# Performance work log

Measured on AMD Instinct MI355X. Metric: run time of the kernel, lower is better.

## Reference

```python
import jax, jax.numpy as jnp
import numpy as np

INPUT_DIM = 1024
LATENT_DIM = 1024


def setup_inputs() -> dict:
    key = jax.random.key(0)
    ks = jax.random.split(key, 8)
    B, T = 64, 512
    concat_dim = INPUT_DIM + LATENT_DIM
    s = lambda fan_in: 1.0 / np.sqrt(fan_in)
    return {
        "x": jax.random.normal(ks[0], (B, T, INPUT_DIM), dtype=jnp.float32),
        "h0": jax.random.normal(ks[1], (B, LATENT_DIM), dtype=jnp.float32),
        "w_W": jax.random.uniform(ks[2], (concat_dim, 2 * LATENT_DIM), jnp.float32, -s(concat_dim), s(concat_dim)),
        "w_b": jax.random.uniform(ks[3], (2 * LATENT_DIM,), jnp.float32, -s(concat_dim), s(concat_dim)),
        "wx_W": jax.random.uniform(ks[4], (INPUT_DIM, LATENT_DIM), jnp.float32, -s(INPUT_DIM), s(INPUT_DIM)),
        "wx_b": jax.random.uniform(ks[5], (LATENT_DIM,), jnp.float32, -s(INPUT_DIM), s(INPUT_DIM)),
        "wh_W": jax.random.uniform(ks[6], (LATENT_DIM, LATENT_DIM), jnp.float32, -s(LATENT_DIM), s(LATENT_DIM)),
        "wh_b": jax.random.uniform(ks[7], (LATENT_DIM,), jnp.float32, -s(LATENT_DIM), s(LATENT_DIM)),
    }


def reference(x, h0, w_W, w_b, wx_W, wx_b, wh_W, wh_b):
    # x: [B, T, D_in] (batch_first). Scan over time.
    xT = jnp.swapaxes(x, 0, 1)  # [T, B, D_in]

    def step(h, x_t):
        # fused gate: sigmoid(cat([x,h]) @ W + b) -> chunk into hidden/output gates
        fused = jax.nn.sigmoid(jnp.concatenate([x_t, h], axis=-1) @ w_W + w_b)
        hidden_state, output_state = jnp.split(fused, 2, axis=-1)
        memory_state = (x_t @ wx_W + wx_b) + hidden_state * (h @ wh_W + wh_b)
        h_new = output_state * h + (1.0 - output_state) * jnp.tanh(memory_state)
        return h_new, h_new

    _, hs = jax.lax.scan(step, h0, xT)  # hs: [T, B, L]
    return jnp.swapaxes(hs, 0, 1)  # [B, T, L]
```

## Files before the change

kernel.cpp:

```cpp
#include <hip/hip_runtime.h>
#include <hip/hip_bf16.h>


typedef __attribute__((ext_vector_type(4))) int   int4v;
typedef __attribute__((ext_vector_type(4))) short short4v;
typedef __attribute__((ext_vector_type(8))) short bf16x8;
typedef __attribute__((ext_vector_type(4))) float f32x4;

union Pack16 { int4v i; short4v s[2]; };
union FragU  { bf16x8 v; short4v s[2]; int4v i; };

__device__ __forceinline__ short f2bf(float f) {
  union { float f; unsigned u; } v; v.f = f;
  unsigned r = v.u + 0x7fffu + ((v.u >> 16) & 1u);
  return (short)(r >> 16);
}
__device__ __forceinline__ float bf2f(short s) {
  union { unsigned u; float f; } v; v.u = ((unsigned)(unsigned short)s) << 16;
  return v.f;
}

#define LDS_BARRIER()                                         \
  do {                                                        \
    asm volatile("s_waitcnt lgkmcnt(0)" ::: "memory");        \
    __builtin_amdgcn_s_barrier();                             \
    asm volatile("" ::: "memory");                            \
  } while (0)

__device__ __forceinline__ void gload_lds16(const short* g, short* l) {
  __builtin_amdgcn_global_load_lds(
      (const __attribute__((address_space(1))) void*)g,
      (__attribute__((address_space(3))) void*)l, 16, 0, 0);
}


__global__ __launch_bounds__(256) void cast_x_kernel(const float* __restrict__ xf,
                                                     short* __restrict__ xbf, int n4) {
  int i = blockIdx.x * 256 + threadIdx.x;
  if (i < n4) {
    float4 v = ((const float4*)xf)[i];
    short4v o;
    o.x = f2bf(v.x); o.y = f2bf(v.y); o.z = f2bf(v.z); o.w = f2bf(v.w);
    int r_in = i >> 8, c = i & 255;
    int b = r_in >> 9, t = r_in & 511;
    ((short4v*)xbf)[((t << 6) + b) * 256 + c] = o;
  }
}

__global__ __launch_bounds__(256) void transpose_cast(const float* __restrict__ src,
                                                      long ld, short* __restrict__ dst) {
  __shared__ float tile[64][65];
  const int n0 = blockIdx.x << 6, k0 = blockIdx.y << 6;
  const int c = threadIdx.x & 63, rr = threadIdx.x >> 6;
#pragma unroll 4
  for (int i = 0; i < 16; ++i)
    tile[i * 4 + rr][c] = src[(long)(k0 + i * 4 + rr) * ld + n0 + c];
  __syncthreads();
#pragma unroll 4
  for (int i = 0; i < 16; ++i)
    dst[(long)(n0 + i * 4 + rr) * 1024 + k0 + c] = f2bf(tile[c][i * 4 + rr]);
}

__global__ __launch_bounds__(256) void prep_misc(const float* __restrict__ wb,
                                                 const float* __restrict__ wxb,
                                                 const float* __restrict__ h0,
                                                 float* __restrict__ biasP,
                                                 short* __restrict__ hbf0) {
  int i = blockIdx.x * 256 + threadIdx.x;
  if (i < 65536) {
    hbf0[i] = f2bf(h0[i]);
  } else {
    int n = i - 65536;
    if (n < 3072) biasP[n] = (n < 2048) ? wb[n] : wxb[n - 2048];
  }
}

__global__ __launch_bounds__(256) void pgemm_kernel(const short* __restrict__ A,
                                                    const short* __restrict__ Bt,
                                                    const float* __restrict__ biasP,
                                                    short* __restrict__ P) {
  __shared__ short As[128][32];
  __shared__ short Bs[128][32];
  const int tid = threadIdx.x;
  const int m0 = blockIdx.y << 7;
  const int n0 = blockIdx.x << 7;
  const int w = tid >> 6, lane = tid & 63;
  const int wm = w >> 1, wn = w & 1;
  const int q = lane >> 4, r = lane & 15;

  const int srow = (w << 5) + (lane >> 2);
  const int scol = (lane & 3) * 8;
  const short* gA0 = A  + (long)(m0 + srow) * 1024 + scol;
  const short* gA1 = gA0 + 16 * 1024;
  const short* gB0 = Bt + (long)(n0 + srow) * 1024 + scol;
  const short* gB1 = gB0 + 16 * 1024;
  short* lA0 = &As[(w << 5)][0];
  short* lA1 = &As[(w << 5) + 16][0];
  short* lB0 = &Bs[(w << 5)][0];
  short* lB1 = &Bs[(w << 5) + 16][0];

  const f32x4 zero = {0.f, 0.f, 0.f, 0.f};
  f32x4 acc[4][4];
#pragma unroll
  for (int a = 0; a < 4; ++a)
#pragma unroll
    for (int b = 0; b < 4; ++b) acc[a][b] = zero;

  for (int kk = 0; kk < 1024; kk += 32) {
    gload_lds16(gA0 + kk, lA0);
    gload_lds16(gA1 + kk, lA1);
    gload_lds16(gB0 + kk, lB0);
    gload_lds16(gB1 + kk, lB1);
    __syncthreads();

    FragU af[4], bfv[4];
#pragma unroll
    for (int mi = 0; mi < 4; ++mi)
      af[mi].i = *(const int4v*)&As[wm * 64 + mi * 16 + r][q * 8];
#pragma unroll
    for (int ni = 0; ni < 4; ++ni)
      bfv[ni].i = *(const int4v*)&Bs[wn * 64 + ni * 16 + r][q * 8];
#pragma unroll
    for (int mi = 0; mi < 4; ++mi)
#pragma unroll
      for (int ni = 0; ni < 4; ++ni)
        acc[mi][ni] = __builtin_amdgcn_mfma_f32_16x16x32_bf16(af[mi].v, bfv[ni].v,
                                                              acc[mi][ni], 0, 0, 0);
    __syncthreads();
  }

#pragma unroll
  for (int ni = 0; ni < 4; ++ni) {
    int gn = n0 + wn * 64 + ni * 16 + r;
    float bias = biasP[gn];
#pragma unroll
    for (int mi = 0; mi < 4; ++mi) {
      int gm = m0 + wm * 64 + mi * 16 + q * 4;
#pragma unroll
      for (int i = 0; i < 4; ++i)
        P[(long)(gm + i) * 3072 + gn] = f2bf(acc[mi][ni][i] + bias);
    }
  }
}

__global__ __launch_bounds__(256, 1) void recur_kernel(const short* __restrict__ RT,
                                                       const short* __restrict__ P,
                                                       const float* __restrict__ whb,
                                                       const float* __restrict__ h0,
                                                       short* __restrict__ hbuf,
                                                       float* __restrict__ out,
                                                       unsigned* __restrict__ sync) {
  __shared__ float Lred[4][3][256];
  __shared__ unsigned long long hstage_u[32];
  short* hstage = (short*)hstage_u;

  const int tid = threadIdx.x;
  const int bid = blockIdx.x;
  const int cg = bid & 63, bg = bid >> 6;
  const int w = tid >> 6, lane = tid & 63;
  const int q = lane >> 4, r = lane & 15;
  const int ks = w << 8;
  const f32x4 zero = {0.f, 0.f, 0.f, 0.f};

  FragU Bf[3][8];
#pragma unroll
  for (int nt = 0; nt < 3; ++nt)
#pragma unroll
    for (int ki = 0; ki < 8; ++ki) {
      const short* p = RT + (long)(nt * 1024 + cg * 16 + r) * 1024 + ks + ki * 32 + q * 8;
      Pack16 t16; t16.i = *(const int4v*)p;
      Bf[nt][ki].s[0] = t16.s[0]; Bf[nt][ki].s[1] = t16.s[1];
    }

  const int bl = tid >> 4, jl = tid & 15;
  float hp = h0[(long)(bg * 16 + bl) * 1024 + cg * 16 + jl];
  const float whbr = whb[cg * 16 + jl];
  const short* Pbase = P + (long)(bg * 16 + bl) * 3072 + cg * 16 + jl;
  short p0n = Pbase[0], p1n = Pbase[1024], p2n = Pbase[2048];
  const long outbase = ((long)(bg * 16 + bl) * 512) * 1024 + cg * 16 + jl;

  unsigned* ctr = sync + bg * 32;
  unsigned* gf  = sync + 128 + bg * 32;

  for (int t = 0; t < 512; ++t) {
    const short* hcur = hbuf + (t & 1) * 65536;
    short* hnext = hbuf + ((t + 1) & 1) * 65536;

    const short* aptr = hcur + (bg * 16 + r) * 1024 + ks + q * 8;
    FragU Af[8];
    asm volatile(
        "global_load_dwordx4 %0, %8, off sc0 sc1\n\t"
        "global_load_dwordx4 %1, %8, off offset:64 sc0 sc1\n\t"
        "global_load_dwordx4 %2, %8, off offset:128 sc0 sc1\n\t"
        "global_load_dwordx4 %3, %8, off offset:192 sc0 sc1\n\t"
        "global_load_dwordx4 %4, %8, off offset:256 sc0 sc1\n\t"
        "global_load_dwordx4 %5, %8, off offset:320 sc0 sc1\n\t"
        "global_load_dwordx4 %6, %8, off offset:384 sc0 sc1\n\t"
        "global_load_dwordx4 %7, %8, off offset:448 sc0 sc1\n\t"
        "s_waitcnt vmcnt(0)"
        : "=&v"(Af[0].i), "=&v"(Af[1].i), "=&v"(Af[2].i), "=&v"(Af[3].i),
          "=&v"(Af[4].i), "=&v"(Af[5].i), "=&v"(Af[6].i), "=&v"(Af[7].i)
        : "v"(aptr)
        : "memory");

    short c0 = p0n, c1 = p1n, c2 = p2n;
    if (t < 511) {
      const short* Pn = Pbase + (long)(t + 1) * 196608;
      p0n = Pn[0]; p1n = Pn[1024]; p2n = Pn[2048];
    }

    f32x4 acc0 = zero, acc1 = zero, acc2 = zero;
#pragma unroll
    for (int ki = 0; ki < 8; ++ki) {
      acc0 = __builtin_amdgcn_mfma_f32_16x16x32_bf16(Af[ki].v, Bf[0][ki].v, acc0, 0, 0, 0);
      acc1 = __builtin_amdgcn_mfma_f32_16x16x32_bf16(Af[ki].v, Bf[1][ki].v, acc1, 0, 0, 0);
      acc2 = __builtin_amdgcn_mfma_f32_16x16x32_bf16(Af[ki].v, Bf[2][ki].v, acc2, 0, 0, 0);
    }

#pragma unroll
    for (int i = 0; i < 4; ++i) {
      Lred[w][0][(q * 4 + i) * 16 + r] = acc0[i];
      Lred[w][1][(q * 4 + i) * 16 + r] = acc1[i];
      Lred[w][2][(q * 4 + i) * 16 + r] = acc2[i];
    }
    LDS_BARRIER();

    float g0 = Lred[0][0][tid] + Lred[1][0][tid] + Lred[2][0][tid] + Lred[3][0][tid];
    float g1 = Lred[0][1][tid] + Lred[1][1][tid] + Lred[2][1][tid] + Lred[3][1][tid];
    float g2 = Lred[0][2][tid] + Lred[1][2][tid] + Lred[2][2][tid] + Lred[3][2][tid];

    float gh = 1.f / (1.f + __expf(-(bf2f(c0) + g0)));
    float go = 1.f / (1.f + __expf(-(bf2f(c1) + g1)));
    float mem = bf2f(c2) + gh * (g2 + whbr);
    float e = __expf(2.f * mem);
    float th = 1.f - 2.f / (e + 1.f);
    float hn = go * hp + (1.f - go) * th;
    hp = hn;
    out[outbase + (long)t * 1024] = hn;
    hstage[tid] = f2bf(hn);
    LDS_BARRIER();

    if (tid < 64) {
      int row = bg * 16 + (tid >> 2);
      unsigned long long* hp64 = (unsigned long long*)(hnext + row * 1024 + cg * 16 + (tid & 3) * 4);
      __hip_atomic_store(hp64, hstage_u[tid], __ATOMIC_RELAXED, __HIP_MEMORY_SCOPE_AGENT);
      asm volatile("s_waitcnt vmcnt(0)" ::: "memory");
      if (tid == 0) {
        unsigned old = __hip_atomic_fetch_add(ctr, 1u, __ATOMIC_RELAXED,
                                              __HIP_MEMORY_SCOPE_AGENT);
        if (old == 64u * (unsigned)(t + 1) - 1u)
          __hip_atomic_store(gf, (unsigned)(t + 1), __ATOMIC_RELAXED,
                             __HIP_MEMORY_SCOPE_AGENT);
      }
      while (__hip_atomic_load(gf, __ATOMIC_RELAXED, __HIP_MEMORY_SCOPE_AGENT) <
             (unsigned)(t + 1))
        __builtin_amdgcn_s_sleep(1);
    }
    LDS_BARRIER();
  }
}


extern "C" void kernel_launch(void* const* d_in, const int* in_sizes, int n_in,
                              void* d_out, int out_size, void* d_ws, size_t ws_size,
                              hipStream_t stream) {
  const float* x   = (const float*)d_in[0];
  const float* h0  = (const float*)d_in[1];
  const float* wW  = (const float*)d_in[2];
  const float* wb  = (const float*)d_in[3];
  const float* wxW = (const float*)d_in[4];
  const float* wxb = (const float*)d_in[5];
  const float* whW = (const float*)d_in[6];
  const float* whb = (const float*)d_in[7];
  float* out = (float*)d_out;

  char* ws = (char*)d_ws;
  short*    P     = (short*)(ws);
  short*    xbf   = (short*)(ws + 201326592);
  short*    XwT   = (short*)(ws + 268435456);
  short*    RT    = (short*)(ws + 274726912);
  float*    biasP = (float*)(ws + 281018368);
  short*    hbf   = (short*)(ws + 281030656);
  unsigned* sync  = (unsigned*)(ws + 281292800);

  hipMemsetAsync(sync, 0, 1024, stream);
  cast_x_kernel<<<dim3(32768), dim3(256), 0, stream>>>(x, xbf, 8388608);
  transpose_cast<<<dim3(32, 16), dim3(256), 0, stream>>>(wW, 2048, XwT);
  transpose_cast<<<dim3(16, 16), dim3(256), 0, stream>>>(wxW, 1024, XwT + 2048 * 1024);
  transpose_cast<<<dim3(32, 16), dim3(256), 0, stream>>>(wW + 1024 * 2048, 2048, RT);
  transpose_cast<<<dim3(16, 16), dim3(256), 0, stream>>>(whW, 1024, RT + 2048 * 1024);
  prep_misc<<<dim3(268), dim3(256), 0, stream>>>(wb, wxb, h0, biasP, hbf);
  pgemm_kernel<<<dim3(24, 256), dim3(256), 0, stream>>>(xbf, XwT, biasP, P);
  recur_kernel<<<dim3(256), dim3(256), 0, stream>>>(RT, P, whb, h0, hbf, out, sync);
}
```

Baseline: 2.490 ms.

## Halve recurrence blocks to 128 with 512 threads sharing h via LDS

The persistent recurrence kernel now runs 128 blocks of 512 threads, each owning 32 hidden columns instead of 16. One wave pair loads the h tile from global memory and shares it through LDS with its partner. The h write-back becomes one 16-byte store per thread, and all threads now spin on the group flag in place of the trailing barrier. Fewer blocks per batch group halve the atomic-counter participants and the redundant global reads of h per step. The cost is an extra LDS barrier per step and more per-block work on the serial critical path.

```diff
diff --git a/kernel.cpp b/kernel.cpp
--- a/kernel.cpp
+++ b/kernel.cpp
@@ -143,41 +143,44 @@
   }
 }
 
-__global__ __launch_bounds__(256, 1) void recur_kernel(const short* __restrict__ RT,
+__global__ __launch_bounds__(512, 1) void recur_kernel(const short* __restrict__ RT,
                                                        const short* __restrict__ P,
                                                        const float* __restrict__ whb,
                                                        const float* __restrict__ h0,
                                                        short* __restrict__ hbuf,
                                                        float* __restrict__ out,
                                                        unsigned* __restrict__ sync) {
-  __shared__ float Lred[4][3][256];
-  __shared__ unsigned long long hstage_u[32];
-  short* hstage = (short*)hstage_u;
+  __shared__ float Lred[4][6][256];
+  __shared__ short Ash[16384];
+  __shared__ short hstage[512];
 
   const int tid = threadIdx.x;
   const int bid = blockIdx.x;
-  const int cg = bid & 63, bg = bid >> 6;
+  const int cg = bid & 31, bg = bid >> 5;
   const int w = tid >> 6, lane = tid & 63;
+  const int kw = w >> 1, cw = w & 1;
   const int q = lane >> 4, r = lane & 15;
-  const int ks = w << 8;
+  const int ks = kw << 8;
   const f32x4 zero = {0.f, 0.f, 0.f, 0.f};
 
   FragU Bf[3][8];
 #pragma unroll
-  for (int nt = 0; nt < 3; ++nt)
+  for (int nt = 0; nt < 3; ++nt) {
+    const long col = nt * 1024 + cg * 32 + cw * 16 + r;
 #pragma unroll
     for (int ki = 0; ki < 8; ++ki) {
-      const short* p = RT + (long)(nt * 1024 + cg * 16 + r) * 1024 + ks + ki * 32 + q * 8;
+      const short* p = RT + col * 1024 + ks + ki * 32 + q * 8;
       Pack16 t16; t16.i = *(const int4v*)p;
       Bf[nt][ki].s[0] = t16.s[0]; Bf[nt][ki].s[1] = t16.s[1];
     }
-
-  const int bl = tid >> 4, jl = tid & 15;
-  float hp = h0[(long)(bg * 16 + bl) * 1024 + cg * 16 + jl];
-  const float whbr = whb[cg * 16 + jl];
-  const short* Pbase = P + (long)(bg * 16 + bl) * 3072 + cg * 16 + jl;
+  }
+
+  const int bl = tid >> 5, jl = tid & 31;
+  float hp = h0[(long)(bg * 16 + bl) * 1024 + cg * 32 + jl];
+  const float whbr = whb[cg * 32 + jl];
+  const short* Pbase = P + (long)(bg * 16 + bl) * 3072 + cg * 32 + jl;
   short p0n = Pbase[0], p1n = Pbase[1024], p2n = Pbase[2048];
-  const long outbase = ((long)(bg * 16 + bl) * 512) * 1024 + cg * 16 + jl;
+  const long outbase = (long)(bg * 16 + bl) * 512 * 1024 + cg * 32 + jl;
 
   unsigned* ctr = sync + bg * 32;
   unsigned* gf  = sync + 128 + bg * 32;
@@ -186,22 +189,28 @@
     const short* hcur = hbuf + (t & 1) * 65536;
     short* hnext = hbuf + ((t + 1) & 1) * 65536;
 
-    const short* aptr = hcur + (bg * 16 + r) * 1024 + ks + q * 8;
     FragU Af[8];
-    asm volatile(
-        "global_load_dwordx4 %0, %8, off sc0 sc1\n\t"
-        "global_load_dwordx4 %1, %8, off offset:64 sc0 sc1\n\t"
-        "global_load_dwordx4 %2, %8, off offset:128 sc0 sc1\n\t"
-        "global_load_dwordx4 %3, %8, off offset:192 sc0 sc1\n\t"
-        "global_load_dwordx4 %4, %8, off offset:256 sc0 sc1\n\t"
-        "global_load_dwordx4 %5, %8, off offset:320 sc0 sc1\n\t"
-        "global_load_dwordx4 %6, %8, off offset:384 sc0 sc1\n\t"
-        "global_load_dwordx4 %7, %8, off offset:448 sc0 sc1\n\t"
-        "s_waitcnt vmcnt(0)"
-        : "=&v"(Af[0].i), "=&v"(Af[1].i), "=&v"(Af[2].i), "=&v"(Af[3].i),
-          "=&v"(Af[4].i), "=&v"(Af[5].i), "=&v"(Af[6].i), "=&v"(Af[7].i)
-        : "v"(aptr)
-        : "memory");
+    if (cw == 0) {
+      const short* aptr = hcur + (bg * 16 + r) * 1024 + ks + q * 8;
+      asm volatile(
+          "global_load_dwordx4 %0, %8, off sc0 sc1\n\t"
+          "global_load_dwordx4 %1, %8, off offset:64 sc0 sc1\n\t"
+          "global_load_dwordx4 %2, %8, off offset:128 sc0 sc1\n\t"
+          "global_load_dwordx4 %3, %8, off offset:192 sc0 sc1\n\t"
+          "global_load_dwordx4 %4, %8, off offset:256 sc0 sc1\n\t"
+          "global_load_dwordx4 %5, %8, off offset:320 sc0 sc1\n\t"
+          "global_load_dwordx4 %6, %8, off offset:384 sc0 sc1\n\t"
+          "global_load_dwordx4 %7, %8, off offset:448 sc0 sc1\n\t"
+          "s_waitcnt vmcnt(0)"
+          : "=&v"(Af[0].i), "=&v"(Af[1].i), "=&v"(Af[2].i), "=&v"(Af[3].i),
+            "=&v"(Af[4].i), "=&v"(Af[5].i), "=&v"(Af[6].i), "=&v"(Af[7].i)
+          : "v"(aptr)
+          : "memory");
+      short* dst = Ash + kw * 4096 + lane * 8;
+#pragma unroll
+      for (int ki = 0; ki < 8; ++ki)
+        *(int4v*)(dst + ki * 512) = Af[ki].i;
+    }
 
     short c0 = p0n, c1 = p1n, c2 = p2n;
     if (t < 511) {
@@ -209,6 +218,15 @@
       p0n = Pn[0]; p1n = Pn[1024]; p2n = Pn[2048];
     }
 
+    LDS_BARRIER();
+
+    if (cw == 1) {
+      const short* src = Ash + kw * 4096 + lane * 8;
+#pragma unroll
+      for (int ki = 0; ki < 8; ++ki)
+        Af[ki].i = *(const int4v*)(src + ki * 512);
+    }
+
     f32x4 acc0 = zero, acc1 = zero, acc2 = zero;
 #pragma unroll
     for (int ki = 0; ki < 8; ++ki) {
@@ -219,21 +237,26 @@
 
 #pragma unroll
     for (int i = 0; i < 4; ++i) {
-      Lred[w][0][(q * 4 + i) * 16 + r] = acc0[i];
-      Lred[w][1][(q * 4 + i) * 16 + r] = acc1[i];
-      Lred[w][2][(q * 4 + i) * 16 + r] = acc2[i];
+      Lred[kw][0 + cw][(q * 4 + i) * 16 + r] = acc0[i];
+      Lred[kw][2 + cw][(q * 4 + i) * 16 + r] = acc1[i];
+      Lred[kw][4 + cw][(q * 4 + i) * 16 + r] = acc2[i];
     }
     LDS_BARRIER();
 
-    float g0 = Lred[0][0][tid] + Lred[1][0][tid] + Lred[2][0][tid] + Lred[3][0][tid];
-    float g1 = Lred[0][1][tid] + Lred[1][1][tid] + Lred[2][1][tid] + Lred[3][1][tid];
-    float g2 = Lred[0][2][tid] + Lred[1][2][tid] + Lred[2][2][tid] + Lred[3][2][tid];
+    const int cwi = jl >> 4, e = bl * 16 + (jl & 15);
+    float g0 = 0.f, g1 = 0.f, g2 = 0.f;
+#pragma unroll
+    for (int kk = 0; kk < 4; ++kk) {
+      g0 += Lred[kk][0 + cwi][e];
+      g1 += Lred[kk][2 + cwi][e];
+      g2 += Lred[kk][4 + cwi][e];
+    }
 
     float gh = 1.f / (1.f + __expf(-(bf2f(c0) + g0)));
     float go = 1.f / (1.f + __expf(-(bf2f(c1) + g1)));
     float mem = bf2f(c2) + gh * (g2 + whbr);
-    float e = __expf(2.f * mem);
-    float th = 1.f - 2.f / (e + 1.f);
+    float e2 = __expf(2.f * mem);
+    float th = 1.f - 2.f / (e2 + 1.f);
     float hn = go * hp + (1.f - go) * th;
     hp = hn;
     out[outbase + (long)t * 1024] = hn;
@@ -241,22 +264,22 @@
     LDS_BARRIER();
 
     if (tid < 64) {
-      int row = bg * 16 + (tid >> 2);
-      unsigned long long* hp64 = (unsigned long long*)(hnext + row * 1024 + cg * 16 + (tid & 3) * 4);
-      __hip_atomic_store(hp64, hstage_u[tid], __ATOMIC_RELAXED, __HIP_MEMORY_SCOPE_AGENT);
+      int4v hd = *(const int4v*)&hstage[tid * 8];
+      short* hap = hnext + (bg * 16 + (tid >> 2)) * 1024 + cg * 32 + (tid & 3) * 8;
+      asm volatile("global_store_dwordx4 %0, %1, off sc0 sc1"
+                   :: "v"(hap), "v"(hd) : "memory");
       asm volatile("s_waitcnt vmcnt(0)" ::: "memory");
       if (tid == 0) {
         unsigned old = __hip_atomic_fetch_add(ctr, 1u, __ATOMIC_RELAXED,
                                               __HIP_MEMORY_SCOPE_AGENT);
-        if (old == 64u * (unsigned)(t + 1) - 1u)
+        if (old == 32u * (unsigned)(t + 1) - 1u)
           __hip_atomic_store(gf, (unsigned)(t + 1), __ATOMIC_RELAXED,
                              __HIP_MEMORY_SCOPE_AGENT);
       }
-      while (__hip_atomic_load(gf, __ATOMIC_RELAXED, __HIP_MEMORY_SCOPE_AGENT) <
-             (unsigned)(t + 1))
-        __builtin_amdgcn_s_sleep(1);
-    }
-    LDS_BARRIER();
+    }
+    while (__hip_atomic_load(gf, __ATOMIC_RELAXED, __HIP_MEMORY_SCOPE_AGENT) <
+           (unsigned)(t + 1))
+      __builtin_amdgcn_s_sleep(1);
   }
 }
 
@@ -291,5 +314,5 @@
   transpose_cast<<<dim3(16, 16), dim3(256), 0, stream>>>(whW, 1024, RT + 2048 * 1024);
   prep_misc<<<dim3(268), dim3(256), 0, stream>>>(wb, wxb, h0, biasP, hbf);
   pgemm_kernel<<<dim3(24, 256), dim3(256), 0, stream>>>(xbf, XwT, biasP, P);
-  recur_kernel<<<dim3(256), dim3(256), 0, stream>>>(RT, P, whb, h0, hbf, out, sync);
-}
+  recur_kernel<<<dim3(128), dim3(512), 0, stream>>>(RT, P, whb, h0, hbf, out, sync);
+}
```

After: 2.504 ms. Within noise of the previous version (+0.6%).
